# Performance work log

Hardware: AMD Instinct MI355X
Metric: run time of the kernel (lower is better)

The kernel has to match this reference:

```python
import jax, jax.numpy as jnp
import numpy as np
import math

D_MODEL = 96
D_STATE = 16
D_CONV = 3
EXPAND = 2
D_INNER = EXPAND * D_MODEL          # 192
DT_RANK = math.ceil(D_MODEL / 16)   # 6
B_SZ, H_SZ, W_SZ = 2, 56, 56


def setup_inputs() -> dict:
    key = jax.random.key(0)
    ks = jax.random.split(key, 10)
    x = jax.random.normal(ks[0], (B_SZ, H_SZ, W_SZ, D_MODEL), jnp.float32)
    W_in = jax.random.normal(ks[1], (D_MODEL, 2 * D_INNER), jnp.float32) * 0.02
    conv_w = jax.random.normal(ks[2], (D_CONV, D_CONV, 1, D_INNER), jnp.float32) * 0.1
    conv_b = jax.random.normal(ks[3], (D_INNER,), jnp.float32) * 0.02
    W_xproj = jax.random.normal(ks[4], (D_INNER, DT_RANK + 2 * D_STATE), jnp.float32) * 0.02
    dt_std = DT_RANK ** -0.5
    W_dt = jax.random.uniform(ks[5], (DT_RANK, D_INNER), jnp.float32, -dt_std, dt_std)
    # dt_proj bias init: inverse-softplus of dt ~ LogUniform(dt_min, dt_max)
    dt_min, dt_max = 1e-3, 1e-1
    dt = jnp.exp(jax.random.uniform(ks[6], (D_INNER,), jnp.float32)
                 * (math.log(dt_max) - math.log(dt_min)) + math.log(dt_min))
    dt = jnp.clip(dt, 1e-4, None)
    b_dt = dt + jnp.log(-jnp.expm1(-dt))
    # A_log initialized to broadcast arange(1..d_state) (as in the source, no log taken)
    A_log = jnp.tile(jnp.arange(1, D_STATE + 1, dtype=jnp.float32)[None, :], (D_INNER, 1))
    D_skip = jnp.ones((D_INNER,), jnp.float32)
    W_out = jax.random.normal(ks[7], (D_INNER, D_MODEL), jnp.float32) * 0.02
    return {"x": x, "W_in": W_in, "conv_w": conv_w, "conv_b": conv_b,
            "W_xproj": W_xproj, "W_dt": W_dt, "b_dt": b_dt,
            "A_log": A_log, "D_skip": D_skip, "W_out": W_out}


def _selective_scan(xs, dt, A, Bm, Cm, D_skip):
    """Canonical Mamba selective scan.
    xs, dt: (G, L, C); Bm, Cm: (G, L, N); A: (C, N); D_skip: (C,).
    h_l = exp(dt_l * A) * h_{l-1} + dt_l * B_l * x_l ;  y_l = <h_l, C_l> + D * x_l
    """
    dA = jnp.exp(dt[..., None] * A)                              # (G,L,C,N)
    dBx = dt[..., None] * Bm[:, :, None, :] * xs[..., None]      # (G,L,C,N)

    def step(h, inp):
        dA_l, dBx_l, C_l = inp                                   # (G,C,N),(G,C,N),(G,N)
        h = dA_l * h + dBx_l
        y = jnp.einsum('gcn,gn->gc', h, C_l)
        return h, y

    G, L, C = xs.shape
    h0 = jnp.zeros((G, C, D_STATE), xs.dtype)
    _, ys = jax.lax.scan(step, h0, (jnp.moveaxis(dA, 1, 0),
                                    jnp.moveaxis(dBx, 1, 0),
                                    jnp.moveaxis(Cm, 1, 0)))
    ys = jnp.moveaxis(ys, 0, 1)                                  # (G,L,C)
    return ys + D_skip * xs


def reference(x, W_in, conv_w, conv_b, W_xproj, W_dt, b_dt, A_log, D_skip, W_out):
    B, H, W, _ = x.shape  # H == W required (source sums transposed scans directly)
    xz = x @ W_in                                                # (B,H,W,2*d_inner)
    xm, z = jnp.split(xz, 2, axis=-1)
    pad = (D_CONV - 1) // 2
    xm = jax.lax.conv_general_dilated(
        xm, conv_w, (1, 1), [(pad, pad), (pad, pad)],
        dimension_numbers=('NHWC', 'HWIO', 'NHWC'),
        feature_group_count=D_INNER) + conv_b                    # depthwise conv
    # 4 scan directions
    xt = jnp.swapaxes(xm, 1, 2)
    xs4 = jnp.stack([xm, jnp.flip(xm, 2), xt, jnp.flip(xt, 1)], 0)  # (4,B,H,W,C)
    G, L = 4 * B, H * W
    xs = xs4.reshape(G, L, D_INNER)
    x_dbl = xs @ W_xproj                                          # (G,L,dt_rank+2N)
    dtr, Bm, Cm = jnp.split(x_dbl, [DT_RANK, DT_RANK + D_STATE], axis=-1)
    dt = jax.nn.softplus(dtr @ W_dt + b_dt)                       # (G,L,d_inner)
    A = -jnp.exp(A_log)                                           # (d_inner, N)
    ys = _selective_scan(xs, dt, A, Bm, Cm, D_skip)               # (G,L,d_inner)
    y = ys.reshape(4, B, H, W, D_INNER).sum(0)                    # sum 4 directions
    y = jax.nn.silu(z) * y
    return y @ W_out                                              # (B,H,W,d_model)
```

## Files before the change

kernel.cpp:

```cpp
#include <hip/hip_runtime.h>
#include <math.h>

#define NPIX 6272
#define LVAL 3136
#define CIN 192
#define NST 16
#define HW 56

__device__ __forceinline__ float softplusf(float v) {
    return (v > 20.0f) ? v : log1pf(expf(v));
}

__device__ __forceinline__ void dir_geom(int d, int b, int& si, int& sj, int& off) {
    if (d == 0)      { si = HW;  sj = 1;   off = b * LVAL; }
    else if (d == 1) { si = HW;  sj = -1;  off = b * LVAL + (HW - 1); }
    else if (d == 2) { si = 1;   sj = HW;  off = b * LVAL; }
    else             { si = -1;  sj = HW;  off = b * LVAL + (HW - 1); }
}

__global__ void k_nop() {}

__global__ __launch_bounds__(384) void k_inproj(
    const float* __restrict__ x, const float* __restrict__ W_in,
    float* __restrict__ xm, float* __restrict__ z)
{
    __shared__ __align__(16) float xs[96][20];
    const int p0 = blockIdx.x * 16;
    const int t = threadIdx.x;
    for (int e = t; e < 16 * 96; e += 384) {
        int p = e / 96, kk = e % 96;
        xs[kk][p] = x[p0 * 96 + e];
    }
    __syncthreads();
    float acc[16];
#pragma unroll
    for (int p = 0; p < 16; ++p) acc[p] = 0.f;
    for (int k = 0; k < 96; ++k) {
        float w = W_in[k * 384 + t];
        float4 x0 = *(const float4*)&xs[k][0];
        float4 x1 = *(const float4*)&xs[k][4];
        float4 x2 = *(const float4*)&xs[k][8];
        float4 x3 = *(const float4*)&xs[k][12];
        acc[0]  = fmaf(x0.x, w, acc[0]);  acc[1]  = fmaf(x0.y, w, acc[1]);
        acc[2]  = fmaf(x0.z, w, acc[2]);  acc[3]  = fmaf(x0.w, w, acc[3]);
        acc[4]  = fmaf(x1.x, w, acc[4]);  acc[5]  = fmaf(x1.y, w, acc[5]);
        acc[6]  = fmaf(x1.z, w, acc[6]);  acc[7]  = fmaf(x1.w, w, acc[7]);
        acc[8]  = fmaf(x2.x, w, acc[8]);  acc[9]  = fmaf(x2.y, w, acc[9]);
        acc[10] = fmaf(x2.z, w, acc[10]); acc[11] = fmaf(x2.w, w, acc[11]);
        acc[12] = fmaf(x3.x, w, acc[12]); acc[13] = fmaf(x3.y, w, acc[13]);
        acc[14] = fmaf(x3.z, w, acc[14]); acc[15] = fmaf(x3.w, w, acc[15]);
    }
#pragma unroll
    for (int p = 0; p < 16; ++p) {
        int pix = p0 + p;
        if (t < 192) xm[pix * CIN + t] = acc[p];
        else         z[pix * CIN + (t - 192)] = acc[p];
    }
}

__global__ __launch_bounds__(512) void k_xproj_dt(
    const float* __restrict__ xm, const float* __restrict__ cw,
    const float* __restrict__ cb,
    const float* __restrict__ W_xproj,
    const float* __restrict__ W_dt, const float* __restrict__ b_dt,
    float* __restrict__ Bp, float* __restrict__ Cp, float2* __restrict__ dtx2)
{
    __shared__ __align__(16) float xs[192][28];
    __shared__ float part[2][24][40];
    __shared__ float dtr_lds[24][8];
    const int p0 = blockIdx.x * 24;
    const int t = threadIdx.x;
    for (int e = t; e < 24 * 192; e += 512) {
        int p = e / 192, kk = e % 192;
        int pix = p0 + p;
        float v = 0.f;
        if (pix < NPIX) {
            int w = pix % HW;
            int rest = pix / HW;
            int h = rest % HW;
            int b = rest / HW;
            v = cb[kk];
#pragma unroll
            for (int ky = 0; ky < 3; ++ky) {
                int hh = h + ky - 1;
                if (hh < 0 || hh >= HW) continue;
#pragma unroll
                for (int kx = 0; kx < 3; ++kx) {
                    int ww = w + kx - 1;
                    if (ww < 0 || ww >= HW) continue;
                    v = fmaf(xm[((b * HW + hh) * HW + ww) * CIN + kk],
                             cw[(ky * 3 + kx) * CIN + kk], v);
                }
            }
        }
        xs[kk][p] = v;
    }
    __syncthreads();
    const int th = t & 255;
    const int kh = t >> 8;
    const int j  = th % 40;
    const int pq = th / 40;
    if (pq < 6) {
        const int jc = (j < 38) ? j : 37;
        float a0 = 0.f, a1 = 0.f, a2 = 0.f, a3 = 0.f;
        const int k0 = kh * 96;
        for (int k = k0; k < k0 + 96; ++k) {
            float w = W_xproj[k * 38 + jc];
            float4 xv = *(const float4*)&xs[k][pq * 4];
            a0 = fmaf(xv.x, w, a0); a1 = fmaf(xv.y, w, a1);
            a2 = fmaf(xv.z, w, a2); a3 = fmaf(xv.w, w, a3);
        }
        part[kh][pq * 4 + 0][j] = a0;
        part[kh][pq * 4 + 1][j] = a1;
        part[kh][pq * 4 + 2][j] = a2;
        part[kh][pq * 4 + 3][j] = a3;
    }
    __syncthreads();
    if (kh == 0 && pq < 6 && j < 38) {
#pragma unroll
        for (int q = 0; q < 4; ++q) {
            int p = pq * 4 + q;
            float r = part[0][p][j] + part[1][p][j];
            int pix = p0 + p;
            if (j < 6) dtr_lds[p][j] = r;
            if (pix < NPIX) {
                if (j < 6)       ;
                else if (j < 22) Bp[pix * NST + (j - 6)] = r;
                else             Cp[pix * NST + (j - 22)] = r;
            }
        }
    }
    __syncthreads();
    for (int e = t; e < 24 * 192; e += 512) {
        int p = e / 192, c = e % 192;
        int pix = p0 + p;
        if (pix >= NPIX) continue;
        float v = b_dt[c];
#pragma unroll
        for (int r = 0; r < 6; ++r)
            v = fmaf(dtr_lds[p][r], W_dt[r * CIN + c], v);
        dtx2[(size_t)pix * CIN + c] = make_float2(softplusf(v), xs[c][p]);
    }
}

template<int CHUNK>
__global__ __launch_bounds__(384) void k_scan_p1(
    const float2* __restrict__ dtx2, const float* __restrict__ Bp,
    const float* __restrict__ A_log,
    float* __restrict__ Pbuf, float* __restrict__ qbuf)
{
    static_assert(CHUNK % 4 == 0, "CHUNK must be multiple of 4");
    constexpr int CPR = HW / CHUNK;
    __shared__ __align__(16) float Bs[CHUNK * NST];
    const int g = blockIdx.y;
    const int k = blockIdx.x;
    const int ch = blockIdx.z;
    const int t = threadIdx.x;
    const int wv = t >> 6;
    const int lane = t & 63;
    const int cl = lane & 15, nh = lane >> 4;
    const int c = ch * 96 + wv * 16 + cl;
    const int n0 = nh * 4;
    const int d = g >> 1, b = g & 1;
    int si, sj, off;
    dir_geom(d, b, si, sj, off);
    const int base = off + (k / CPR) * si + ((k % CPR) * CHUNK) * sj;

    for (int e = t; e < CHUNK * NST; e += 384) {
        int jj = e >> 4, n = e & 15;
        Bs[e] = Bp[(base + jj * sj) * NST + n];
    }

    const float LOG2E = 1.4426950408889634f;
    float a2[4];
    {
        float4 v = *(const float4*)(A_log + c * NST + n0);
        a2[0] = -expf(v.x) * LOG2E;
        a2[1] = -expf(v.y) * LOG2E;
        a2[2] = -expf(v.z) * LOG2E;
        a2[3] = -expf(v.w) * LOG2E;
    }
    __syncthreads();

    float h[4];
#pragma unroll
    for (int i = 0; i < 4; ++i) h[i] = 0.f;
    float Sdt = 0.f;

    const float2* dp = dtx2 + (size_t)base * CIN + c;
    const ptrdiff_t dstep = (ptrdiff_t)sj * CIN;

#define P1_STEP(DVV, JJ) do {                                            \
        float dt_c = (DVV).x, x_c = (DVV).y;                             \
        float dtx = dt_c * x_c;                                          \
        Sdt += dt_c;                                                     \
        float4 t0 = *(const float4*)(Bs + (JJ) * NST + n0);              \
        float Bv[4] = {t0.x, t0.y, t0.z, t0.w};                          \
        _Pragma("unroll")                                                \
        for (int i = 0; i < 4; ++i) {                                    \
            float dA = exp2f(dt_c * a2[i]);                              \
            h[i] = fmaf(dA, h[i], dtx * Bv[i]);                          \
        }                                                                \
    } while (0)

    float2 v0 = dp[0];
    float2 v1 = dp[dstep];
    float2 v2 = dp[2 * dstep];
    float2 v3 = dp[3 * dstep];
    for (int jj = 0; jj < CHUNK; jj += 4) {
        const int j4 = (jj + 4 < CHUNK) ? jj + 4 : CHUNK - 4;
        float2 nv0 = dp[(ptrdiff_t)(j4 + 0) * dstep];
        float2 nv1 = dp[(ptrdiff_t)(j4 + 1) * dstep];
        float2 nv2 = dp[(ptrdiff_t)(j4 + 2) * dstep];
        float2 nv3 = dp[(ptrdiff_t)(j4 + 3) * dstep];
        P1_STEP(v0, jj + 0);
        P1_STEP(v1, jj + 1);
        P1_STEP(v2, jj + 2);
        P1_STEP(v3, jj + 3);
        v0 = nv0; v1 = nv1; v2 = nv2; v3 = nv3;
    }
#undef P1_STEP

    float P[4];
#pragma unroll
    for (int i = 0; i < 4; ++i) P[i] = exp2f(a2[i] * Sdt);

    float4* Pd = (float4*)(Pbuf + ((size_t)(k * 8 + g) * CIN + c) * NST + n0);
    float4* qd = (float4*)(qbuf + ((size_t)(k * 8 + g) * CIN + c) * NST + n0);
    Pd[0] = make_float4(P[0], P[1], P[2], P[3]);
    qd[0] = make_float4(h[0], h[1], h[2], h[3]);
}

__global__ __launch_bounds__(256) void k_scan_fix(
    const float* __restrict__ Pbuf, float* __restrict__ qbuf, int nch)
{
    const int g = blockIdx.y;
    const int lo = blockIdx.x * 256 + threadIdx.x;
    const size_t stride = (size_t)8 * CIN * NST;
    size_t idx  = (size_t)g * CIN * NST + lo;
    size_t pidx = idx;
    float Pr[8], qr[8];
#pragma unroll
    for (int i = 0; i < 8; ++i) { Pr[i] = Pbuf[pidx]; qr[i] = qbuf[pidx]; pidx += stride; }
    float h = 0.f;
    for (int k = 0; k < nch; k += 8) {
        float Pn[8], qn[8];
        if (k + 8 < nch) {
#pragma unroll
            for (int i = 0; i < 8; ++i) {
                Pn[i] = Pbuf[pidx + (size_t)i * stride];
                qn[i] = qbuf[pidx + (size_t)i * stride];
            }
        } else {
#pragma unroll
            for (int i = 0; i < 8; ++i) { Pn[i] = 0.f; qn[i] = 0.f; }
        }
#pragma unroll
        for (int i = 0; i < 8; ++i) {
            qbuf[idx] = h;
            h = fmaf(Pr[i], h, qr[i]);
            idx += stride;
        }
#pragma unroll
        for (int i = 0; i < 8; ++i) { Pr[i] = Pn[i]; qr[i] = qn[i]; }
        pidx += (size_t)8 * stride;
    }
}

template<int CHUNK>
__global__ __launch_bounds__(384) void k_scan_p2(
    const float2* __restrict__ dtx2, const float* __restrict__ Bp,
    const float* __restrict__ Cp, const float* __restrict__ A_log,
    const float* __restrict__ D_skip,
    const float* __restrict__ qbuf, float* __restrict__ Y4)
{
    static_assert(CHUNK % 4 == 0, "CHUNK must be multiple of 4");
    constexpr int CPR = HW / CHUNK;
    __shared__ __align__(16) float Bs[CHUNK * NST];
    __shared__ __align__(16) float Cs[CHUNK * NST];
    const int g = blockIdx.y;
    const int k = blockIdx.x;
    const int ch = blockIdx.z;
    const int t = threadIdx.x;
    const int wv = t >> 6;
    const int lane = t & 63;
    const int cl = lane & 15, nh = lane >> 4;
    const int c = ch * 96 + wv * 16 + cl;
    const int n0 = nh * 4;
    const int d = g >> 1, b = g & 1;
    int si, sj, off;
    dir_geom(d, b, si, sj, off);
    const int base = off + (k / CPR) * si + ((k % CPR) * CHUNK) * sj;

    for (int e = t; e < CHUNK * NST; e += 384) {
        int jj = e >> 4, n = e & 15;
        int pa = (base + jj * sj) * NST + n;
        Bs[e] = Bp[pa];
        Cs[e] = Cp[pa];
    }

    const float LOG2E = 1.4426950408889634f;
    float a2[4];
    {
        float4 v = *(const float4*)(A_log + c * NST + n0);
        a2[0] = -expf(v.x) * LOG2E;
        a2[1] = -expf(v.y) * LOG2E;
        a2[2] = -expf(v.z) * LOG2E;
        a2[3] = -expf(v.w) * LOG2E;
    }
    const float Dc = D_skip[c];

    float h[4];
    {
        float4 v0q = *(const float4*)(qbuf + ((size_t)(k * 8 + g) * CIN + c) * NST + n0);
        h[0]=v0q.x; h[1]=v0q.y; h[2]=v0q.z; h[3]=v0q.w;
    }
    __syncthreads();

    float* yo = Y4 + ((size_t)d * NPIX + (size_t)b * LVAL + (size_t)k * CHUNK) * CIN;

    const float2* dp = dtx2 + (size_t)base * CIN + c;
    const ptrdiff_t dstep = (ptrdiff_t)sj * CIN;

#define P2_STEP(DVV, JJ) do {                                            \
        float dt_c = (DVV).x, x_c = (DVV).y;                             \
        float dtx = dt_c * x_c;                                          \
        float4 t0 = *(const float4*)(Bs + (JJ) * NST + n0);              \
        float4 u0 = *(const float4*)(Cs + (JJ) * NST + n0);              \
        float Bv[4] = {t0.x, t0.y, t0.z, t0.w};                          \
        float Cv[4] = {u0.x, u0.y, u0.z, u0.w};                          \
        float yc0 = 0.f, yc1 = 0.f;                                      \
        _Pragma("unroll")                                                \
        for (int i = 0; i < 4; i += 2) {                                 \
            float dA0 = exp2f(dt_c * a2[i]);                             \
            float dA1 = exp2f(dt_c * a2[i+1]);                           \
            h[i]   = fmaf(dA0, h[i],   dtx * Bv[i]);                     \
            h[i+1] = fmaf(dA1, h[i+1], dtx * Bv[i+1]);                   \
            yc0 = fmaf(h[i],   Cv[i],   yc0);                            \
            yc1 = fmaf(h[i+1], Cv[i+1], yc1);                            \
        }                                                                \
        float yc = yc0 + yc1;                                            \
        yc += __shfl_xor(yc, 16, 64);                                    \
        yc += __shfl_xor(yc, 32, 64);                                    \
        if (nh == 0)                                                     \
            yo[(JJ) * CIN + c] = fmaf(Dc, x_c, yc);                      \
    } while (0)

    float2 v0 = dp[0];
    float2 v1 = dp[dstep];
    float2 v2 = dp[2 * dstep];
    float2 v3 = dp[3 * dstep];
    for (int jj = 0; jj < CHUNK; jj += 4) {
        const int j4 = (jj + 4 < CHUNK) ? jj + 4 : CHUNK - 4;
        float2 nv0 = dp[(ptrdiff_t)(j4 + 0) * dstep];
        float2 nv1 = dp[(ptrdiff_t)(j4 + 1) * dstep];
        float2 nv2 = dp[(ptrdiff_t)(j4 + 2) * dstep];
        float2 nv3 = dp[(ptrdiff_t)(j4 + 3) * dstep];
        P2_STEP(v0, jj + 0);
        P2_STEP(v1, jj + 1);
        P2_STEP(v2, jj + 2);
        P2_STEP(v3, jj + 3);
        v0 = nv0; v1 = nv1; v2 = nv2; v3 = nv3;
    }
#undef P2_STEP
}

__global__ __launch_bounds__(384) void k_gateout(
    const float* __restrict__ Y4, const float* __restrict__ z,
    const float* __restrict__ W_out, float* __restrict__ out)
{
    __shared__ __align__(16) float xs[192][20];
    const int p0 = blockIdx.x * 16;
    const int t = threadIdx.x;
    const size_t NP = (size_t)NPIX * CIN;
    for (int e = t; e < 16 * 192; e += 384) {
        int p = e / 192, c = e % 192;
        size_t idx = (size_t)(p0 + p) * CIN + c;
        float s = Y4[idx] + Y4[idx + NP] + Y4[idx + 2 * NP] + Y4[idx + 3 * NP];
        float zz = z[idx];
        float sig = 1.f / (1.f + expf(-zz));
        xs[c][p] = zz * sig * s;
    }
    __syncthreads();
    const int j  = t % 96;
    const int ph = t / 96;
    float acc[4] = {0.f, 0.f, 0.f, 0.f};
    for (int k = 0; k < 192; ++k) {
        float w = W_out[k * 96 + j];
        float4 xv = *(const float4*)&xs[k][ph * 4];
        acc[0] = fmaf(xv.x, w, acc[0]); acc[1] = fmaf(xv.y, w, acc[1]);
        acc[2] = fmaf(xv.z, w, acc[2]); acc[3] = fmaf(xv.w, w, acc[3]);
    }
#pragma unroll
    for (int p = 0; p < 4; ++p)
        out[(p0 + ph * 4 + p) * 96 + j] = acc[p];
}

template<int CHUNK>
static void launch_scan(const float2* dtx2, const float* Bp, const float* Cp,
                        const float* A_log, const float* D_skip,
                        float* Pbuf, float* qbuf, float* Y4, hipStream_t stream)
{
    const int nch = LVAL / CHUNK;
    k_scan_p1<CHUNK><<<dim3(nch, 8, 2), 384, 0, stream>>>(dtx2, Bp, A_log, Pbuf, qbuf);
    k_scan_fix<<<dim3(12, 8), 256, 0, stream>>>(Pbuf, qbuf, nch);
    k_scan_p2<CHUNK><<<dim3(nch, 8, 2), 384, 0, stream>>>(dtx2, Bp, Cp, A_log, D_skip, qbuf, Y4);
}

extern "C" void kernel_launch(void* const* d_in, const int* in_sizes, int n_in,
                              void* d_out, int out_size, void* d_ws, size_t ws_size,
                              hipStream_t stream) {
    const float* x      = (const float*)d_in[0];
    const float* W_in   = (const float*)d_in[1];
    const float* conv_w = (const float*)d_in[2];
    const float* conv_b = (const float*)d_in[3];
    const float* W_xproj= (const float*)d_in[4];
    const float* W_dt   = (const float*)d_in[5];
    const float* b_dt   = (const float*)d_in[6];
    const float* A_log  = (const float*)d_in[7];
    const float* D_skip = (const float*)d_in[8];
    const float* W_out  = (const float*)d_in[9];
    float* out = (float*)d_out;

    float* ws   = (float*)d_ws;
    float* xm   = ws;
    float* z    = xm  + NPIX * CIN;
    float* xcv  = z   + NPIX * CIN;
    float2* dtx2= (float2*)(xcv + NPIX * CIN);
    float* Bp   = (float*)(dtx2 + (size_t)NPIX * CIN);
    float* Cp   = Bp  + NPIX * NST;
    float* Y4   = Cp  + NPIX * NST;
    float* Pbuf = Y4  + (size_t)4 * NPIX * CIN;

    const size_t base_fl = 11038720;
    const size_t ws_fl = ws_size / 4;
    int chunk;
    if (ws_fl >= base_fl + (size_t)2 * 112 * 24576) chunk = 28;
    else                                            chunk = 56;
    float* qbuf = Pbuf + (size_t)(LVAL / chunk) * 8 * CIN * NST;

    k_inproj  <<<NPIX / 16, 384, 0, stream>>>(x, W_in, xm, z);
    k_xproj_dt<<<(NPIX + 23) / 24, 512, 0, stream>>>(xm, conv_w, conv_b,
                                                     W_xproj, W_dt, b_dt, Bp, Cp, dtx2);
    if (chunk == 28) launch_scan<28>(dtx2, Bp, Cp, A_log, D_skip, Pbuf, qbuf, Y4, stream);
    else             launch_scan<56>(dtx2, Bp, Cp, A_log, D_skip, Pbuf, qbuf, Y4, stream);
    k_gateout <<<NPIX / 16, 384, 0, stream>>>(Y4, z, W_out, out);

    for (int rep = 0; rep < 20; ++rep)
        k_nop<<<1, 64, 0, stream>>>();
}
```

Baseline: 241.3 us.

## Replace two-pass chunked scan with local scan plus closed-form carry correction

The scan no longer recomputes the recurrence in a second pass. The first kernel now runs the chunk scan from a zero state and writes both the local outputs and the running dt sums. A new correction kernel adds C·exp(A·cumdt)·h_carry using the carries fixed up between chunks. The change also drops the trailing no-op launches and the workspace-dependent chunk choice. In exchange it writes and reads an extra per-element dt-sum buffer, does a read-modify-write of Y4, and assumes the workspace is large enough for chunk size 28.

```diff
diff --git a/kernel.cpp b/kernel.cpp
--- a/kernel.cpp
+++ b/kernel.cpp
@@ -6,6 +6,8 @@
 #define CIN 192
 #define NST 16
 #define HW 56
+#define CHUNK28 28
+#define NCH 112
 
 __device__ __forceinline__ float softplusf(float v) {
     return (v > 20.0f) ? v : log1pf(expf(v));
@@ -17,8 +19,6 @@
     else if (d == 2) { si = 1;   sj = HW;  off = b * LVAL; }
     else             { si = -1;  sj = HW;  off = b * LVAL + (HW - 1); }
 }
-
-__global__ void k_nop() {}
 
 __global__ __launch_bounds__(384) void k_inproj(
     const float* __restrict__ x, const float* __restrict__ W_in,
@@ -143,15 +143,16 @@
     }
 }
 
-template<int CHUNK>
-__global__ __launch_bounds__(384) void k_scan_p1(
+__global__ __launch_bounds__(384) void k_scan_y(
     const float2* __restrict__ dtx2, const float* __restrict__ Bp,
-    const float* __restrict__ A_log,
-    float* __restrict__ Pbuf, float* __restrict__ qbuf)
-{
-    static_assert(CHUNK % 4 == 0, "CHUNK must be multiple of 4");
-    constexpr int CPR = HW / CHUNK;
-    __shared__ __align__(16) float Bs[CHUNK * NST];
+    const float* __restrict__ Cp, const float* __restrict__ A_log,
+    const float* __restrict__ D_skip,
+    float* __restrict__ Pbuf, float* __restrict__ qbuf,
+    float* __restrict__ Sbuf, float* __restrict__ Y4)
+{
+    constexpr int CPR = HW / CHUNK28;
+    __shared__ __align__(16) float Bs[CHUNK28 * NST];
+    __shared__ __align__(16) float Cs[CHUNK28 * NST];
     const int g = blockIdx.y;
     const int k = blockIdx.x;
     const int ch = blockIdx.z;
@@ -164,11 +165,13 @@
     const int d = g >> 1, b = g & 1;
     int si, sj, off;
     dir_geom(d, b, si, sj, off);
-    const int base = off + (k / CPR) * si + ((k % CPR) * CHUNK) * sj;
-
-    for (int e = t; e < CHUNK * NST; e += 384) {
+    const int base = off + (k / CPR) * si + ((k % CPR) * CHUNK28) * sj;
+
+    for (int e = t; e < CHUNK28 * NST; e += 384) {
         int jj = e >> 4, n = e & 15;
-        Bs[e] = Bp[(base + jj * sj) * NST + n];
+        int pa = (base + jj * sj) * NST + n;
+        Bs[e] = Bp[pa];
+        Cs[e] = Cp[pa];
     }
 
     const float LOG2E = 1.4426950408889634f;
@@ -180,54 +183,45 @@
         a2[2] = -expf(v.z) * LOG2E;
         a2[3] = -expf(v.w) * LOG2E;
     }
-    __syncthreads();
-
-    float h[4];
-#pragma unroll
-    for (int i = 0; i < 4; ++i) h[i] = 0.f;
-    float Sdt = 0.f;
+    const float Dc = D_skip[c];
+    __syncthreads();
+
+    float* yo = Y4   + ((size_t)g * LVAL + (size_t)k * CHUNK28) * CIN;
+    float* So = Sbuf + ((size_t)g * LVAL + (size_t)k * CHUNK28) * CIN;
 
     const float2* dp = dtx2 + (size_t)base * CIN + c;
     const ptrdiff_t dstep = (ptrdiff_t)sj * CIN;
 
-#define P1_STEP(DVV, JJ) do {                                            \
-        float dt_c = (DVV).x, x_c = (DVV).y;                             \
-        float dtx = dt_c * x_c;                                          \
-        Sdt += dt_c;                                                     \
-        float4 t0 = *(const float4*)(Bs + (JJ) * NST + n0);              \
-        float Bv[4] = {t0.x, t0.y, t0.z, t0.w};                          \
-        _Pragma("unroll")                                                \
-        for (int i = 0; i < 4; ++i) {                                    \
-            float dA = exp2f(dt_c * a2[i]);                              \
-            h[i] = fmaf(dA, h[i], dtx * Bv[i]);                          \
-        }                                                                \
-    } while (0)
-
-    float2 v0 = dp[0];
-    float2 v1 = dp[dstep];
-    float2 v2 = dp[2 * dstep];
-    float2 v3 = dp[3 * dstep];
-    for (int jj = 0; jj < CHUNK; jj += 4) {
-        const int j4 = (jj + 4 < CHUNK) ? jj + 4 : CHUNK - 4;
-        float2 nv0 = dp[(ptrdiff_t)(j4 + 0) * dstep];
-        float2 nv1 = dp[(ptrdiff_t)(j4 + 1) * dstep];
-        float2 nv2 = dp[(ptrdiff_t)(j4 + 2) * dstep];
-        float2 nv3 = dp[(ptrdiff_t)(j4 + 3) * dstep];
-        P1_STEP(v0, jj + 0);
-        P1_STEP(v1, jj + 1);
-        P1_STEP(v2, jj + 2);
-        P1_STEP(v3, jj + 3);
-        v0 = nv0; v1 = nv1; v2 = nv2; v3 = nv3;
-    }
-#undef P1_STEP
-
-    float P[4];
-#pragma unroll
-    for (int i = 0; i < 4; ++i) P[i] = exp2f(a2[i] * Sdt);
+    float h[4] = {0.f, 0.f, 0.f, 0.f};
+    float Sdt = 0.f;
+    float2 dv = dp[0];
+    for (int jj = 0; jj < CHUNK28; ++jj) {
+        float dt_c = dv.x, x_c = dv.y;
+        int jn = (jj + 1 < CHUNK28) ? jj + 1 : jj;
+        dv = dp[(ptrdiff_t)jn * dstep];
+        float dtx = dt_c * x_c;
+        Sdt += dt_c;
+        float4 t0 = *(const float4*)(Bs + jj * NST + n0);
+        float4 u0 = *(const float4*)(Cs + jj * NST + n0);
+        float yc = 0.f;
+#pragma unroll
+        for (int i = 0; i < 4; ++i) {
+            float dA = exp2f(dt_c * a2[i]);
+            h[i] = fmaf(dA, h[i], (&t0.x)[i] * dtx);
+            yc = fmaf(h[i], (&u0.x)[i], yc);
+        }
+        yc += __shfl_xor(yc, 16, 64);
+        yc += __shfl_xor(yc, 32, 64);
+        if (nh == 0) {
+            yo[jj * CIN + c] = fmaf(Dc, x_c, yc);
+            So[jj * CIN + c] = Sdt;
+        }
+    }
 
     float4* Pd = (float4*)(Pbuf + ((size_t)(k * 8 + g) * CIN + c) * NST + n0);
     float4* qd = (float4*)(qbuf + ((size_t)(k * 8 + g) * CIN + c) * NST + n0);
-    Pd[0] = make_float4(P[0], P[1], P[2], P[3]);
+    Pd[0] = make_float4(exp2f(a2[0]*Sdt), exp2f(a2[1]*Sdt),
+                        exp2f(a2[2]*Sdt), exp2f(a2[3]*Sdt));
     qd[0] = make_float4(h[0], h[1], h[2], h[3]);
 }
 
@@ -267,102 +261,61 @@
     }
 }
 
-template<int CHUNK>
-__global__ __launch_bounds__(384) void k_scan_p2(
-    const float2* __restrict__ dtx2, const float* __restrict__ Bp,
+__global__ __launch_bounds__(384) void k_scan_corr(
+    const float* __restrict__ qbuf,
     const float* __restrict__ Cp, const float* __restrict__ A_log,
-    const float* __restrict__ D_skip,
-    const float* __restrict__ qbuf, float* __restrict__ Y4)
-{
-    static_assert(CHUNK % 4 == 0, "CHUNK must be multiple of 4");
-    constexpr int CPR = HW / CHUNK;
-    __shared__ __align__(16) float Bs[CHUNK * NST];
-    __shared__ __align__(16) float Cs[CHUNK * NST];
+    const float* __restrict__ Sbuf, float* __restrict__ Y4)
+{
+    __shared__ __align__(16) float qs[CIN * NST];
+    __shared__ __align__(16) float as[CIN * NST];
+    __shared__ __align__(16) float cs[CHUNK28 * NST];
+    const int k = blockIdx.x;
     const int g = blockIdx.y;
-    const int k = blockIdx.x;
-    const int ch = blockIdx.z;
-    const int t = threadIdx.x;
-    const int wv = t >> 6;
-    const int lane = t & 63;
-    const int cl = lane & 15, nh = lane >> 4;
-    const int c = ch * 96 + wv * 16 + cl;
-    const int n0 = nh * 4;
-    const int d = g >> 1, b = g & 1;
-    int si, sj, off;
-    dir_geom(d, b, si, sj, off);
-    const int base = off + (k / CPR) * si + ((k % CPR) * CHUNK) * sj;
-
-    for (int e = t; e < CHUNK * NST; e += 384) {
-        int jj = e >> 4, n = e & 15;
-        int pa = (base + jj * sj) * NST + n;
-        Bs[e] = Bp[pa];
-        Cs[e] = Cp[pa];
-    }
-
+    const int t = threadIdx.x;
     const float LOG2E = 1.4426950408889634f;
-    float a2[4];
+    const size_t qbase = (size_t)(k * 8 + g) * CIN * NST;
+    for (int e = t; e < CIN * NST; e += 384) {
+        qs[e] = qbuf[qbase + e];
+        as[e] = -expf(A_log[e]) * LOG2E;
+    }
     {
-        float4 v = *(const float4*)(A_log + c * NST + n0);
-        a2[0] = -expf(v.x) * LOG2E;
-        a2[1] = -expf(v.y) * LOG2E;
-        a2[2] = -expf(v.z) * LOG2E;
-        a2[3] = -expf(v.w) * LOG2E;
-    }
-    const float Dc = D_skip[c];
-
-    float h[4];
-    {
-        float4 v0q = *(const float4*)(qbuf + ((size_t)(k * 8 + g) * CIN + c) * NST + n0);
-        h[0]=v0q.x; h[1]=v0q.y; h[2]=v0q.z; h[3]=v0q.w;
-    }
-    __syncthreads();
-
-    float* yo = Y4 + ((size_t)d * NPIX + (size_t)b * LVAL + (size_t)k * CHUNK) * CIN;
-
-    const float2* dp = dtx2 + (size_t)base * CIN + c;
-    const ptrdiff_t dstep = (ptrdiff_t)sj * CIN;
-
-#define P2_STEP(DVV, JJ) do {                                            \
-        float dt_c = (DVV).x, x_c = (DVV).y;                             \
-        float dtx = dt_c * x_c;                                          \
-        float4 t0 = *(const float4*)(Bs + (JJ) * NST + n0);              \
-        float4 u0 = *(const float4*)(Cs + (JJ) * NST + n0);              \
-        float Bv[4] = {t0.x, t0.y, t0.z, t0.w};                          \
-        float Cv[4] = {u0.x, u0.y, u0.z, u0.w};                          \
-        float yc0 = 0.f, yc1 = 0.f;                                      \
-        _Pragma("unroll")                                                \
-        for (int i = 0; i < 4; i += 2) {                                 \
-            float dA0 = exp2f(dt_c * a2[i]);                             \
-            float dA1 = exp2f(dt_c * a2[i+1]);                           \
-            h[i]   = fmaf(dA0, h[i],   dtx * Bv[i]);                     \
-            h[i+1] = fmaf(dA1, h[i+1], dtx * Bv[i+1]);                   \
-            yc0 = fmaf(h[i],   Cv[i],   yc0);                            \
-            yc1 = fmaf(h[i+1], Cv[i+1], yc1);                            \
-        }                                                                \
-        float yc = yc0 + yc1;                                            \
-        yc += __shfl_xor(yc, 16, 64);                                    \
-        yc += __shfl_xor(yc, 32, 64);                                    \
-        if (nh == 0)                                                     \
-            yo[(JJ) * CIN + c] = fmaf(Dc, x_c, yc);                      \
-    } while (0)
-
-    float2 v0 = dp[0];
-    float2 v1 = dp[dstep];
-    float2 v2 = dp[2 * dstep];
-    float2 v3 = dp[3 * dstep];
-    for (int jj = 0; jj < CHUNK; jj += 4) {
-        const int j4 = (jj + 4 < CHUNK) ? jj + 4 : CHUNK - 4;
-        float2 nv0 = dp[(ptrdiff_t)(j4 + 0) * dstep];
-        float2 nv1 = dp[(ptrdiff_t)(j4 + 1) * dstep];
-        float2 nv2 = dp[(ptrdiff_t)(j4 + 2) * dstep];
-        float2 nv3 = dp[(ptrdiff_t)(j4 + 3) * dstep];
-        P2_STEP(v0, jj + 0);
-        P2_STEP(v1, jj + 1);
-        P2_STEP(v2, jj + 2);
-        P2_STEP(v3, jj + 3);
-        v0 = nv0; v1 = nv1; v2 = nv2; v3 = nv3;
-    }
-#undef P2_STEP
+        const int d = g >> 1, b = g & 1;
+        int si, sj, off; dir_geom(d, b, si, sj, off);
+        for (int e = t; e < CHUNK28 * NST; e += 384) {
+            int jl = e >> 4, n = e & 15;
+            int l = k * CHUNK28 + jl;
+            int i = l / 56, j = l % 56;
+            int pix = off + i * si + j * sj;
+            cs[e] = Cp[pix * NST + n];
+        }
+    }
+    __syncthreads();
+    const int c  = t % 192;
+    const int jh = t / 192;
+    float4 qv[4], av[4];
+#pragma unroll
+    for (int q = 0; q < 4; ++q) {
+        qv[q] = *(const float4*)(qs + c * NST + q * 4);
+        av[q] = *(const float4*)(as + c * NST + q * 4);
+    }
+    const size_t fb = ((size_t)g * LVAL + (size_t)k * CHUNK28) * CIN + c;
+#pragma unroll
+    for (int m = 0; m < 14; ++m) {
+        const int jl = jh * 14 + m;
+        const size_t flat = fb + (size_t)jl * CIN;
+        float S = Sbuf[flat];
+        float y = Y4[flat];
+        float corr = 0.f;
+#pragma unroll
+        for (int q = 0; q < 4; ++q) {
+            float4 cv = *(const float4*)(cs + jl * NST + q * 4);
+            corr = fmaf(cv.x * qv[q].x, exp2f(av[q].x * S), corr);
+            corr = fmaf(cv.y * qv[q].y, exp2f(av[q].y * S), corr);
+            corr = fmaf(cv.z * qv[q].z, exp2f(av[q].z * S), corr);
+            corr = fmaf(cv.w * qv[q].w, exp2f(av[q].w * S), corr);
+        }
+        Y4[flat] = y + corr;
+    }
 }
 
 __global__ __launch_bounds__(384) void k_gateout(
@@ -394,17 +347,6 @@
 #pragma unroll
     for (int p = 0; p < 4; ++p)
         out[(p0 + ph * 4 + p) * 96 + j] = acc[p];
-}
-
-template<int CHUNK>
-static void launch_scan(const float2* dtx2, const float* Bp, const float* Cp,
-                        const float* A_log, const float* D_skip,
-                        float* Pbuf, float* qbuf, float* Y4, hipStream_t stream)
-{
-    const int nch = LVAL / CHUNK;
-    k_scan_p1<CHUNK><<<dim3(nch, 8, 2), 384, 0, stream>>>(dtx2, Bp, A_log, Pbuf, qbuf);
-    k_scan_fix<<<dim3(12, 8), 256, 0, stream>>>(Pbuf, qbuf, nch);
-    k_scan_p2<CHUNK><<<dim3(nch, 8, 2), 384, 0, stream>>>(dtx2, Bp, Cp, A_log, D_skip, qbuf, Y4);
 }
 
 extern "C" void kernel_launch(void* const* d_in, const int* in_sizes, int n_in,
@@ -431,21 +373,15 @@
     float* Cp   = Bp  + NPIX * NST;
     float* Y4   = Cp  + NPIX * NST;
     float* Pbuf = Y4  + (size_t)4 * NPIX * CIN;
-
-    const size_t base_fl = 11038720;
-    const size_t ws_fl = ws_size / 4;
-    int chunk;
-    if (ws_fl >= base_fl + (size_t)2 * 112 * 24576) chunk = 28;
-    else                                            chunk = 56;
-    float* qbuf = Pbuf + (size_t)(LVAL / chunk) * 8 * CIN * NST;
+    float* qbuf = Pbuf + (size_t)NCH * 8 * CIN * NST;
+    float* Sbuf = qbuf + (size_t)NCH * 8 * CIN * NST;
 
     k_inproj  <<<NPIX / 16, 384, 0, stream>>>(x, W_in, xm, z);
     k_xproj_dt<<<(NPIX + 23) / 24, 512, 0, stream>>>(xm, conv_w, conv_b,
                                                      W_xproj, W_dt, b_dt, Bp, Cp, dtx2);
-    if (chunk == 28) launch_scan<28>(dtx2, Bp, Cp, A_log, D_skip, Pbuf, qbuf, Y4, stream);
-    else             launch_scan<56>(dtx2, Bp, Cp, A_log, D_skip, Pbuf, qbuf, Y4, stream);
-    k_gateout <<<NPIX / 16, 384, 0, stream>>>(Y4, z, W_out, out);
-
-    for (int rep = 0; rep < 20; ++rep)
-        k_nop<<<1, 64, 0, stream>>>();
-}
+    k_scan_y   <<<dim3(NCH, 8, 2), 384, 0, stream>>>(dtx2, Bp, Cp, A_log, D_skip,
+                                                     Pbuf, qbuf, Sbuf, Y4);
+    k_scan_fix <<<dim3(12, 8), 256, 0, stream>>>(Pbuf, qbuf, NCH);
+    k_scan_corr<<<dim3(NCH, 8), 384, 0, stream>>>(qbuf, Cp, A_log, Sbuf, Y4);
+    k_gateout  <<<NPIX / 16, 384, 0, stream>>>(Y4, z, W_out, out);
+}
```

After: 217.5 us. 9.9% less time.

## Store per-chunk dt sums instead of decay products and drop dummy launches

Applied to the files above, without the earlier changes.

The first scan pass now writes one summed dt per (chunk, group, channel) instead of 16 precomputed decay factors per state. The fix-up kernel recomputes the decay with exp2 from A_log, which cuts intermediate buffer traffic. The chunk size is fixed at 28, so the workspace-size check and the template dispatch are gone. The 20 trailing empty kernel launches are removed, and a no-op FMA is inserted in the input-projection loop. The cost is extra exp2 work in the serial fix-up loop.

```diff
diff --git a/kernel.cpp b/kernel.cpp
--- a/kernel.cpp
+++ b/kernel.cpp
@@ -6,6 +6,8 @@
 #define CIN 192
 #define NST 16
 #define HW 56
+#define CHUNK 28
+#define NCH 112
 
 __device__ __forceinline__ float softplusf(float v) {
     return (v > 20.0f) ? v : log1pf(expf(v));
@@ -17,8 +19,6 @@
     else if (d == 2) { si = 1;   sj = HW;  off = b * LVAL; }
     else             { si = -1;  sj = HW;  off = b * LVAL + (HW - 1); }
 }
-
-__global__ void k_nop() {}
 
 __global__ __launch_bounds__(384) void k_inproj(
     const float* __restrict__ x, const float* __restrict__ W_in,
@@ -47,7 +47,8 @@
         acc[6]  = fmaf(x1.z, w, acc[6]);  acc[7]  = fmaf(x1.w, w, acc[7]);
         acc[8]  = fmaf(x2.x, w, acc[8]);  acc[9]  = fmaf(x2.y, w, acc[9]);
         acc[10] = fmaf(x2.z, w, acc[10]); acc[11] = fmaf(x2.w, w, acc[11]);
-        acc[12] = fmaf(x3.x, w, acc[12]); acc[13] = fmaf(x3.y, w, acc[13]);
+        acc[12] = fmaf(x3.x, w, acc[12]); acc[13] = fmaf(x3.w ? x3.x : x3.x, 0.f, acc[13]);
+        acc[13] = fmaf(x3.y, w, acc[13]);
         acc[14] = fmaf(x3.z, w, acc[14]); acc[15] = fmaf(x3.w, w, acc[15]);
     }
 #pragma unroll
@@ -143,13 +144,11 @@
     }
 }
 
-template<int CHUNK>
 __global__ __launch_bounds__(384) void k_scan_p1(
     const float2* __restrict__ dtx2, const float* __restrict__ Bp,
     const float* __restrict__ A_log,
-    float* __restrict__ Pbuf, float* __restrict__ qbuf)
-{
-    static_assert(CHUNK % 4 == 0, "CHUNK must be multiple of 4");
+    float* __restrict__ Sd, float* __restrict__ qbuf)
+{
     constexpr int CPR = HW / CHUNK;
     __shared__ __align__(16) float Bs[CHUNK * NST];
     const int g = blockIdx.y;
@@ -221,60 +220,65 @@
     }
 #undef P1_STEP
 
-    float P[4];
-#pragma unroll
-    for (int i = 0; i < 4; ++i) P[i] = exp2f(a2[i] * Sdt);
-
-    float4* Pd = (float4*)(Pbuf + ((size_t)(k * 8 + g) * CIN + c) * NST + n0);
+    if (nh == 0)
+        Sd[(size_t)(k * 8 + g) * CIN + c] = Sdt;
     float4* qd = (float4*)(qbuf + ((size_t)(k * 8 + g) * CIN + c) * NST + n0);
-    Pd[0] = make_float4(P[0], P[1], P[2], P[3]);
     qd[0] = make_float4(h[0], h[1], h[2], h[3]);
 }
 
 __global__ __launch_bounds__(256) void k_scan_fix(
-    const float* __restrict__ Pbuf, float* __restrict__ qbuf, int nch)
+    const float* __restrict__ Sd, const float* __restrict__ A_log,
+    float* __restrict__ qbuf, int nch)
 {
     const int g = blockIdx.y;
     const int lo = blockIdx.x * 256 + threadIdx.x;
+    const int c = lo >> 4;
+    const float LOG2E = 1.4426950408889634f;
+    const float a2t = -expf(A_log[lo]) * LOG2E;
     const size_t stride = (size_t)8 * CIN * NST;
+    const size_t sstride = (size_t)8 * CIN;
     size_t idx  = (size_t)g * CIN * NST + lo;
     size_t pidx = idx;
-    float Pr[8], qr[8];
-#pragma unroll
-    for (int i = 0; i < 8; ++i) { Pr[i] = Pbuf[pidx]; qr[i] = qbuf[pidx]; pidx += stride; }
+    size_t sidx = (size_t)g * CIN + c;
+    float Sv[8], qr[8];
+#pragma unroll
+    for (int i = 0; i < 8; ++i) {
+        Sv[i] = Sd[sidx]; qr[i] = qbuf[pidx];
+        sidx += sstride; pidx += stride;
+    }
     float h = 0.f;
     for (int k = 0; k < nch; k += 8) {
-        float Pn[8], qn[8];
+        float Sn[8], qn[8];
         if (k + 8 < nch) {
 #pragma unroll
             for (int i = 0; i < 8; ++i) {
-                Pn[i] = Pbuf[pidx + (size_t)i * stride];
+                Sn[i] = Sd[sidx + (size_t)i * sstride];
                 qn[i] = qbuf[pidx + (size_t)i * stride];
             }
         } else {
 #pragma unroll
-            for (int i = 0; i < 8; ++i) { Pn[i] = 0.f; qn[i] = 0.f; }
+            for (int i = 0; i < 8; ++i) { Sn[i] = 0.f; qn[i] = 0.f; }
         }
 #pragma unroll
         for (int i = 0; i < 8; ++i) {
             qbuf[idx] = h;
-            h = fmaf(Pr[i], h, qr[i]);
+            float P = exp2f(a2t * Sv[i]);
+            h = fmaf(P, h, qr[i]);
             idx += stride;
         }
 #pragma unroll
-        for (int i = 0; i < 8; ++i) { Pr[i] = Pn[i]; qr[i] = qn[i]; }
+        for (int i = 0; i < 8; ++i) { Sv[i] = Sn[i]; qr[i] = qn[i]; }
+        sidx += (size_t)8 * sstride;
         pidx += (size_t)8 * stride;
     }
 }
 
-template<int CHUNK>
 __global__ __launch_bounds__(384) void k_scan_p2(
     const float2* __restrict__ dtx2, const float* __restrict__ Bp,
     const float* __restrict__ Cp, const float* __restrict__ A_log,
     const float* __restrict__ D_skip,
     const float* __restrict__ qbuf, float* __restrict__ Y4)
 {
-    static_assert(CHUNK % 4 == 0, "CHUNK must be multiple of 4");
     constexpr int CPR = HW / CHUNK;
     __shared__ __align__(16) float Bs[CHUNK * NST];
     __shared__ __align__(16) float Cs[CHUNK * NST];
@@ -396,17 +400,6 @@
         out[(p0 + ph * 4 + p) * 96 + j] = acc[p];
 }
 
-template<int CHUNK>
-static void launch_scan(const float2* dtx2, const float* Bp, const float* Cp,
-                        const float* A_log, const float* D_skip,
-                        float* Pbuf, float* qbuf, float* Y4, hipStream_t stream)
-{
-    const int nch = LVAL / CHUNK;
-    k_scan_p1<CHUNK><<<dim3(nch, 8, 2), 384, 0, stream>>>(dtx2, Bp, A_log, Pbuf, qbuf);
-    k_scan_fix<<<dim3(12, 8), 256, 0, stream>>>(Pbuf, qbuf, nch);
-    k_scan_p2<CHUNK><<<dim3(nch, 8, 2), 384, 0, stream>>>(dtx2, Bp, Cp, A_log, D_skip, qbuf, Y4);
-}
-
 extern "C" void kernel_launch(void* const* d_in, const int* in_sizes, int n_in,
                               void* d_out, int out_size, void* d_ws, size_t ws_size,
                               hipStream_t stream) {
@@ -430,22 +423,14 @@
     float* Bp   = (float*)(dtx2 + (size_t)NPIX * CIN);
     float* Cp   = Bp  + NPIX * NST;
     float* Y4   = Cp  + NPIX * NST;
-    float* Pbuf = Y4  + (size_t)4 * NPIX * CIN;
-
-    const size_t base_fl = 11038720;
-    const size_t ws_fl = ws_size / 4;
-    int chunk;
-    if (ws_fl >= base_fl + (size_t)2 * 112 * 24576) chunk = 28;
-    else                                            chunk = 56;
-    float* qbuf = Pbuf + (size_t)(LVAL / chunk) * 8 * CIN * NST;
+    float* Sd   = Y4  + (size_t)4 * NPIX * CIN;
+    float* qbuf = Sd  + (size_t)NCH * 8 * CIN;
 
     k_inproj  <<<NPIX / 16, 384, 0, stream>>>(x, W_in, xm, z);
     k_xproj_dt<<<(NPIX + 23) / 24, 512, 0, stream>>>(xm, conv_w, conv_b,
                                                      W_xproj, W_dt, b_dt, Bp, Cp, dtx2);
-    if (chunk == 28) launch_scan<28>(dtx2, Bp, Cp, A_log, D_skip, Pbuf, qbuf, Y4, stream);
-    else             launch_scan<56>(dtx2, Bp, Cp, A_log, D_skip, Pbuf, qbuf, Y4, stream);
+    k_scan_p1 <<<dim3(NCH, 8, 2), 384, 0, stream>>>(dtx2, Bp, A_log, Sd, qbuf);
+    k_scan_fix<<<dim3(12, 8), 256, 0, stream>>>(Sd, A_log, qbuf, NCH);
+    k_scan_p2 <<<dim3(NCH, 8, 2), 384, 0, stream>>>(dtx2, Bp, Cp, A_log, D_skip, qbuf, Y4);
     k_gateout <<<NPIX / 16, 384, 0, stream>>>(Y4, z, W_out, out);
-
-    for (int rep = 0; rep < 20; ++rep)
-        k_nop<<<1, 64, 0, stream>>>();
-}
+}
```

Result: faster. 211.7 us (-12.2%).
